# Optimization experiments

Hardware: AMD Instinct MI355X
Metric: run time of the kernel (lower is better)

The kernel has to match this reference:

```python
import jax, jax.numpy as jnp
import numpy as np

B, T, S, D_MODEL = 2, 16, 512, 768
N_HEADS, HEAD_DIM = 12, 64
N_LATENTS = 32


def build_encoder_mask(modality_ids, n_latents):
    # encoder mode: latent queries attend everything; non-latent queries attend same-modality only
    S = modality_ids.shape[0]
    is_q_lat = (jnp.arange(S) < n_latents)[:, None]            # (S,1)
    same_mod = modality_ids[:, None] == modality_ids[None, :]  # (S,S)
    return jnp.where(is_q_lat, True, same_mod)                 # (S,S) bool


def setup_inputs() -> dict:
    key = jax.random.key(0)
    ks = jax.random.split(key, 9)
    x = jax.random.normal(ks[0], (B, T, S, D_MODEL), jnp.float32)
    w_scale = 1.0 / np.sqrt(D_MODEL)
    # flax MultiHeadDotProductAttention param layout: qkv kernels (D, H, head_dim), out kernel (H, head_dim, D)
    Wq = jax.random.normal(ks[1], (D_MODEL, N_HEADS, HEAD_DIM), jnp.float32) * w_scale
    Wk = jax.random.normal(ks[2], (D_MODEL, N_HEADS, HEAD_DIM), jnp.float32) * w_scale
    Wv = jax.random.normal(ks[3], (D_MODEL, N_HEADS, HEAD_DIM), jnp.float32) * w_scale
    Wo = jax.random.normal(ks[4], (N_HEADS, HEAD_DIM, D_MODEL), jnp.float32) * w_scale
    bq = jnp.zeros((N_HEADS, HEAD_DIM), jnp.float32)
    bk = jnp.zeros((N_HEADS, HEAD_DIM), jnp.float32)
    bv = jnp.zeros((N_HEADS, HEAD_DIM), jnp.float32)
    bo = jnp.zeros((D_MODEL,), jnp.float32)
    # 32 latent tokens (id -1), then 240 tokens of modality 0 and 240 of modality 1
    modality_ids = jnp.concatenate([
        jnp.full((N_LATENTS,), -1, jnp.int32),
        jnp.zeros((240,), jnp.int32),
        jnp.ones((240,), jnp.int32),
    ])
    return dict(x=x, Wq=Wq, bq=bq, Wk=Wk, bk=bk, Wv=Wv, bv=bv, Wo=Wo, bo=bo,
                modality_ids=modality_ids, n_latents=N_LATENTS)


def reference(x, Wq, bq, Wk, bk, Wv, bv, Wo, bo, modality_ids, n_latents):
    B, T, S, D = x.shape
    H, hd = Wq.shape[1], Wq.shape[2]
    xf = x.reshape(B * T, S, D)                                   # (BT,S,D)
    q = (jnp.einsum('bsd,dhk->bshk', xf, Wq) + bq) / jnp.sqrt(jnp.asarray(hd, x.dtype))
    k = jnp.einsum('bsd,dhk->bshk', xf, Wk) + bk
    v = jnp.einsum('bsd,dhk->bshk', xf, Wv) + bv
    scores = jnp.einsum('bqhd,bkhd->bhqk', q, k)                  # (BT,H,S,S)
    mask = build_encoder_mask(modality_ids, n_latents)            # (S,S)
    neg = jnp.finfo(x.dtype).min
    scores = jnp.where(mask[None, None], scores, neg)
    attn = jax.nn.softmax(scores, axis=-1)
    ctx = jnp.einsum('bhqk,bkhd->bqhd', attn, v)                  # (BT,S,H,hd)
    y = jnp.einsum('bqhd,hdo->bqo', ctx, Wo) + bo                 # (BT,S,D)
    return y.reshape(B, T, S, D)
```

## Files before the change

kernel.cpp:

```cpp
#include <hip/hip_runtime.h>
#include <stdint.h>

#define BT_N  32
#define SEQL  512
#define DM    768
#define NHEAD 12
#define HDIM  64
#define MTOT  (BT_N * SEQL)

typedef __bf16 bf16x8 __attribute__((ext_vector_type(8)));
typedef float  f32x4  __attribute__((ext_vector_type(4)));

__device__ __forceinline__ float b2f(uint16_t u)  { return __uint_as_float(((uint32_t)u) << 16); }
__device__ __forceinline__ uint16_t f2b(float f) {
    uint32_t u = __float_as_uint(f);
    return (uint16_t)((u + 0x7fffu + ((u >> 16) & 1u)) >> 16);
}
__device__ __forceinline__ void split_bf16(float x, uint16_t& hi, uint16_t& lo) {
    hi = f2b(x);
    lo = f2b(x - b2f(hi));
}

__device__ __forceinline__ void gload16(const void* g, void* l) {
    __builtin_amdgcn_global_load_lds(
        (const __attribute__((address_space(1))) void*)g,
        (__attribute__((address_space(3))) void*)l,
        16, 0, 0);
}

__global__ __launch_bounds__(256) void split_x_kernel(
    const float* __restrict__ X, uint16_t* __restrict__ Xh, uint16_t* __restrict__ Xl)
{
    size_t i = ((size_t)blockIdx.x * 256 + threadIdx.x) * 4;
    float4 v = *(const float4*)(X + i);
    float xx[4] = {v.x, v.y, v.z, v.w};
    ushort4 h, l;
    uint16_t hh, ll;
    split_bf16(xx[0], hh, ll); h.x = hh; l.x = ll;
    split_bf16(xx[1], hh, ll); h.y = hh; l.y = ll;
    split_bf16(xx[2], hh, ll); h.z = hh; l.z = ll;
    split_bf16(xx[3], hh, ll); h.w = hh; l.w = ll;
    *(ushort4*)(Xh + i) = h;
    *(ushort4*)(Xl + i) = l;
}

__global__ __launch_bounds__(256) void wprep_kernel(
    const float* __restrict__ Wq, const float* __restrict__ Wk,
    const float* __restrict__ Wv, const float* __restrict__ Wo,
    uint16_t* __restrict__ WqTh, uint16_t* __restrict__ WqTl,
    uint16_t* __restrict__ WkTh, uint16_t* __restrict__ WkTl,
    uint16_t* __restrict__ WvT,  uint16_t* __restrict__ WoT)
{
    __shared__ float tile[32][33];
    const int z = blockIdx.z;
    const float* W; uint16_t* Th; uint16_t* Tl;
    if (z == 0)      { W = Wq; Th = WqTh; Tl = WqTl; }
    else if (z == 1) { W = Wk; Th = WkTh; Tl = WkTl; }
    else if (z == 2) { W = Wv; Th = WvT;  Tl = nullptr; }
    else             { W = Wo; Th = WoT;  Tl = nullptr; }

    const int k0 = blockIdx.x * 32, n0 = blockIdx.y * 32;
    const int tid = threadIdx.x;
    {
        int r = tid >> 3, c = (tid & 7) * 4;
        *(float4*)&tile[r][c] = *(const float4*)(W + (size_t)(k0 + r) * DM + n0 + c);
    }
    __syncthreads();
    {
        int nl = tid >> 3, kk = (tid & 7) * 4;
        ushort4 h, l;
        uint16_t hh, ll;
        float v0 = tile[kk + 0][nl], v1 = tile[kk + 1][nl];
        float v2 = tile[kk + 2][nl], v3 = tile[kk + 3][nl];
        split_bf16(v0, hh, ll); h.x = hh; l.x = ll;
        split_bf16(v1, hh, ll); h.y = hh; l.y = ll;
        split_bf16(v2, hh, ll); h.z = hh; l.z = ll;
        split_bf16(v3, hh, ll); h.w = hh; l.w = ll;
        size_t o = (size_t)(n0 + nl) * DM + k0 + kk;
        *(ushort4*)(Th + o) = h;
        if (Tl) *(ushort4*)(Tl + o) = l;
    }
}

__global__ __launch_bounds__(256, 2) void qk_gemm_split(
    const uint16_t* __restrict__ Xh, const uint16_t* __restrict__ Xl,
    const uint16_t* __restrict__ WqTh, const uint16_t* __restrict__ WqTl,
    const uint16_t* __restrict__ WkTh, const uint16_t* __restrict__ WkTl,
    const float* __restrict__ bq, const float* __restrict__ bk,
    uint16_t* __restrict__ Qh, uint16_t* __restrict__ Ql,
    uint16_t* __restrict__ Kh, uint16_t* __restrict__ Kl)
{
    __shared__ uint16_t lds[2][16384];

    const int m0 = blockIdx.x * 128;
    const int n0 = blockIdx.y * 128;
    const int z  = blockIdx.z;

    const uint16_t* Bh_g = z ? WkTh : WqTh;
    const uint16_t* Bl_g = z ? WkTl : WqTl;
    const float* bias    = z ? bk : bq;
    uint16_t* OutH       = z ? Kh : Qh;
    uint16_t* OutL       = z ? Kl : Ql;
    const float scale    = z ? 1.0f : 0.125f;

    const int tid  = threadIdx.x;
    const int lane = tid & 63, wave = tid >> 6;
    const int quad = lane >> 4, l16 = lane & 15;
    const int wm = (wave >> 1) * 64, wn = (wave & 1) * 64;

    const uint16_t* src[8];
    #pragma unroll
    for (int i = 0; i < 8; i++) {
        int d    = (i * 256 + tid) * 16;
        int row  = (d >> 7) & 127;
        int colb = d & 127;
        int scol = colb ^ ((row & 7) << 4);
        int kofs = (scol & 63) >> 1;
        const uint16_t* g;
        if (d < 16384) g = (scol < 64 ? Xh : Xl)     + (size_t)(m0 + row) * DM + kofs;
        else           g = (scol < 64 ? Bh_g : Bl_g) + (size_t)(n0 + row) * DM + kofs;
        src[i] = g;
    }

    int offA[4], offB[4];
    #pragma unroll
    for (int i = 0; i < 4; i++) {
        int r  = wm + i * 16 + l16;
        offA[i] = r * 64 + (((quad * 16) ^ ((r & 7) << 4)) >> 1);
        int rb = wn + i * 16 + l16;
        offB[i] = 8192 + rb * 64 + (((quad * 16) ^ ((rb & 7) << 4)) >> 1);
    }

    f32x4 acc[4][4];
    #pragma unroll
    for (int i = 0; i < 4; i++)
        #pragma unroll
        for (int j = 0; j < 4; j++) acc[i][j] = (f32x4){0.f,0.f,0.f,0.f};

    auto stage = [&](int buf) {
        #pragma unroll
        for (int i = 0; i < 8; i++) {
            gload16(src[i], &lds[buf][(i * 256 + wave * 64) * 8]);
            src[i] += 32;
        }
    };
    auto computeTile = [&](int buf) {
        const uint16_t* base = &lds[buf][0];
        bf16x8 ah[4], al[4], bh[4], bl[4];
        #pragma unroll
        for (int i = 0; i < 4; i++) {
            ah[i] = *(const bf16x8*)(base + offA[i]);
            al[i] = *(const bf16x8*)(base + (offA[i] ^ 32));
            bh[i] = *(const bf16x8*)(base + offB[i]);
            bl[i] = *(const bf16x8*)(base + (offB[i] ^ 32));
        }
        #pragma unroll
        for (int mi = 0; mi < 4; mi++)
            #pragma unroll
            for (int ni = 0; ni < 4; ni++) {
                acc[mi][ni] = __builtin_amdgcn_mfma_f32_16x16x32_bf16(al[mi], bh[ni], acc[mi][ni], 0, 0, 0);
                acc[mi][ni] = __builtin_amdgcn_mfma_f32_16x16x32_bf16(ah[mi], bl[ni], acc[mi][ni], 0, 0, 0);
                acc[mi][ni] = __builtin_amdgcn_mfma_f32_16x16x32_bf16(ah[mi], bh[ni], acc[mi][ni], 0, 0, 0);
            }
    };

    stage(0);
    asm volatile("s_waitcnt vmcnt(0)" ::: "memory");
    __syncthreads();

    int cur = 0;
    for (int t = 0; t < 23; t++) {
        stage(cur ^ 1);
        computeTile(cur);
        asm volatile("s_waitcnt vmcnt(0)" ::: "memory");
        __syncthreads();
        cur ^= 1;
    }
    computeTile(cur);

    #pragma unroll
    for (int i = 0; i < 4; i++) {
        #pragma unroll
        for (int j = 0; j < 4; j++) {
            int n = n0 + wn + j * 16 + l16;
            float bsv = bias[n];
            int hh = n >> 6, dd = n & 63;
            int mb = m0 + wm + i * 16 + quad * 4;
            #pragma unroll
            for (int r = 0; r < 4; r++) {
                int m = mb + r;
                float val = (acc[i][j][r] + bsv) * scale;
                uint16_t vh, vl; split_bf16(val, vh, vl);
                int bt = m >> 9, s = m & 511;
                size_t idx = (((size_t)bt * NHEAD + hh) * SEQL + s) * HDIM + dd;
                OutH[idx] = vh; OutL[idx] = vl;
            }
        }
    }
}

__global__ __launch_bounds__(256, 2) void v_gemm_plain(
    const uint16_t* __restrict__ Xh, const uint16_t* __restrict__ WvT,
    const float* __restrict__ bv, uint16_t* __restrict__ Vt)
{
    __shared__ uint16_t lds[2][16384];

    const int m0 = blockIdx.x * 128;
    const int n0 = blockIdx.y * 128;
    const int tid  = threadIdx.x;
    const int lane = tid & 63, wave = tid >> 6;
    const int quad = lane >> 4, l16 = lane & 15;
    const int wm = (wave >> 1) * 64, wn = (wave & 1) * 64;

    const uint16_t* src[8];
    #pragma unroll
    for (int i = 0; i < 8; i++) {
        int d    = (i * 256 + tid) * 16;
        int row  = (d >> 7) & 127;
        int colb = d & 127;
        int scol = colb ^ ((row & 7) << 4);
        int kofs = scol >> 1;
        src[i] = (d < 16384 ? Xh + (size_t)(m0 + row) * DM
                            : WvT + (size_t)(n0 + row) * DM) + kofs;
    }

    int offA[4], offB[4];
    #pragma unroll
    for (int i = 0; i < 4; i++) {
        int r  = wm + i * 16 + l16;
        offA[i] = r * 64 + (((quad * 16) ^ ((r & 7) << 4)) >> 1);
        int rb = wn + i * 16 + l16;
        offB[i] = 8192 + rb * 64 + (((quad * 16) ^ ((rb & 7) << 4)) >> 1);
    }

    f32x4 acc[4][4];
    #pragma unroll
    for (int i = 0; i < 4; i++)
        #pragma unroll
        for (int j = 0; j < 4; j++) acc[i][j] = (f32x4){0.f,0.f,0.f,0.f};

    auto stage = [&](int buf) {
        #pragma unroll
        for (int i = 0; i < 8; i++) {
            gload16(src[i], &lds[buf][(i * 256 + wave * 64) * 8]);
            src[i] += 64;
        }
    };
    auto computeTile = [&](int buf) {
        const uint16_t* base = &lds[buf][0];
        bf16x8 a0[4], a1[4], b0[4], b1[4];
        #pragma unroll
        for (int i = 0; i < 4; i++) {
            a0[i] = *(const bf16x8*)(base + offA[i]);
            a1[i] = *(const bf16x8*)(base + (offA[i] ^ 32));
            b0[i] = *(const bf16x8*)(base + offB[i]);
            b1[i] = *(const bf16x8*)(base + (offB[i] ^ 32));
        }
        #pragma unroll
        for (int mi = 0; mi < 4; mi++)
            #pragma unroll
            for (int ni = 0; ni < 4; ni++)
                acc[mi][ni] = __builtin_amdgcn_mfma_f32_16x16x32_bf16(a0[mi], b0[ni], acc[mi][ni], 0, 0, 0);
        #pragma unroll
        for (int mi = 0; mi < 4; mi++)
            #pragma unroll
            for (int ni = 0; ni < 4; ni++)
                acc[mi][ni] = __builtin_amdgcn_mfma_f32_16x16x32_bf16(a1[mi], b1[ni], acc[mi][ni], 0, 0, 0);
    };

    stage(0);
    asm volatile("s_waitcnt vmcnt(0)" ::: "memory");
    __syncthreads();

    int cur = 0;
    for (int t = 0; t < 11; t++) {
        stage(cur ^ 1);
        computeTile(cur);
        asm volatile("s_waitcnt vmcnt(0)" ::: "memory");
        __syncthreads();
        cur ^= 1;
    }
    computeTile(cur);

    #pragma unroll
    for (int i = 0; i < 4; i++) {
        #pragma unroll
        for (int j = 0; j < 4; j++) {
            int n = n0 + wn + j * 16 + l16;
            float bsv = bv[n];
            int hh = n >> 6, dd = n & 63;
            int mb = m0 + wm + i * 16 + quad * 4;
            int bt = mb >> 9, sb = mb & 511;
            ushort4 pk;
            pk.x = f2b(acc[i][j][0] + bsv);
            pk.y = f2b(acc[i][j][1] + bsv);
            pk.z = f2b(acc[i][j][2] + bsv);
            pk.w = f2b(acc[i][j][3] + bsv);
            *(ushort4*)&Vt[(((size_t)bt * NHEAD + hh) * HDIM + dd) * SEQL + sb] = pk;
        }
    }
}

__global__ __launch_bounds__(256, 2) void out_proj_v3(
    const uint16_t* __restrict__ A, const uint16_t* __restrict__ WoT,
    const float* __restrict__ bias, float* __restrict__ Y)
{
    __shared__ uint16_t lds[2][16384];

    const int m0 = blockIdx.x * 128;
    const int n0 = blockIdx.y * 128;
    const int tid  = threadIdx.x;
    const int lane = tid & 63, wave = tid >> 6;
    const int quad = lane >> 4, l16 = lane & 15;
    const int wm = (wave >> 1) * 64, wn = (wave & 1) * 64;

    const uint16_t* src[8];
    #pragma unroll
    for (int i = 0; i < 8; i++) {
        int d    = (i * 256 + tid) * 16;
        int row  = (d >> 7) & 127;
        int colb = d & 127;
        int scol = colb ^ ((row & 7) << 4);
        int kofs = scol >> 1;
        src[i] = (d < 16384 ? A + (size_t)(m0 + row) * DM
                            : WoT + (size_t)(n0 + row) * DM) + kofs;
    }

    int offA[4], offB[4];
    #pragma unroll
    for (int i = 0; i < 4; i++) {
        int r  = wm + i * 16 + l16;
        offA[i] = r * 64 + (((quad * 16) ^ ((r & 7) << 4)) >> 1);
        int rb = wn + i * 16 + l16;
        offB[i] = 8192 + rb * 64 + (((quad * 16) ^ ((rb & 7) << 4)) >> 1);
    }

    f32x4 acc[4][4];
    #pragma unroll
    for (int i = 0; i < 4; i++)
        #pragma unroll
        for (int j = 0; j < 4; j++) acc[i][j] = (f32x4){0.f,0.f,0.f,0.f};

    auto stage = [&](int buf) {
        #pragma unroll
        for (int i = 0; i < 8; i++) {
            gload16(src[i], &lds[buf][(i * 256 + wave * 64) * 8]);
            src[i] += 64;
        }
    };
    auto computeTile = [&](int buf) {
        const uint16_t* base = &lds[buf][0];
        bf16x8 a0[4], a1[4], b0[4], b1[4];
        #pragma unroll
        for (int i = 0; i < 4; i++) {
            a0[i] = *(const bf16x8*)(base + offA[i]);
            a1[i] = *(const bf16x8*)(base + (offA[i] ^ 32));
            b0[i] = *(const bf16x8*)(base + offB[i]);
            b1[i] = *(const bf16x8*)(base + (offB[i] ^ 32));
        }
        #pragma unroll
        for (int mi = 0; mi < 4; mi++)
            #pragma unroll
            for (int ni = 0; ni < 4; ni++)
                acc[mi][ni] = __builtin_amdgcn_mfma_f32_16x16x32_bf16(a0[mi], b0[ni], acc[mi][ni], 0, 0, 0);
        #pragma unroll
        for (int mi = 0; mi < 4; mi++)
            #pragma unroll
            for (int ni = 0; ni < 4; ni++)
                acc[mi][ni] = __builtin_amdgcn_mfma_f32_16x16x32_bf16(a1[mi], b1[ni], acc[mi][ni], 0, 0, 0);
    };

    stage(0);
    asm volatile("s_waitcnt vmcnt(0)" ::: "memory");
    __syncthreads();

    int cur = 0;
    for (int t = 0; t < 11; t++) {
        stage(cur ^ 1);
        computeTile(cur);
        asm volatile("s_waitcnt vmcnt(0)" ::: "memory");
        __syncthreads();
        cur ^= 1;
    }
    computeTile(cur);

    #pragma unroll
    for (int i = 0; i < 4; i++) {
        #pragma unroll
        for (int j = 0; j < 4; j++) {
            int n = n0 + wn + j * 16 + l16;
            float bsv = bias[n];
            int mb = m0 + wm + i * 16 + quad * 4;
            #pragma unroll
            for (int r = 0; r < 4; r++)
                Y[(size_t)(mb + r) * DM + n] = acc[i][j][r] + bsv;
        }
    }
}

#define QTILE 64

__global__ __launch_bounds__(256) void attn_mfma_v2(
    const uint16_t* __restrict__ Qhg, const uint16_t* __restrict__ Qlg,
    const uint16_t* __restrict__ Khg, const uint16_t* __restrict__ Klg,
    const uint16_t* __restrict__ Vtg, const int* __restrict__ modality,
    const int* __restrict__ nlat_p, uint16_t* __restrict__ ctx)
{
    __shared__ uint16_t KhS[64][72];
    __shared__ uint16_t KlS[64][72];
    __shared__ uint16_t Vs[64][72];
    __shared__ __bf16   Ps[QTILE][72];
    __shared__ int modk_s[64];

    const int bh = blockIdx.x;
    const int bt = bh / NHEAD, h = bh % NHEAD;
    const int q0 = blockIdx.y * QTILE;
    const int tid = threadIdx.x, lane = tid & 63, wave = tid >> 6;
    const int quad = lane >> 4, l16 = lane & 15;
    const int wq = wave * 16;

    const size_t hb = (size_t)bh * SEQL * HDIM;
    const int nlat = nlat_p[0];

    unsigned needmask;
    {
        int rm = modality[q0 + lane];
        bool hasLat = __any((q0 + lane) < nlat);
        bool has0   = __any(rm == 0);
        bool has1   = __any(rm == 1);
        needmask = 0;
        #pragma unroll
        for (int t8 = 0; t8 < 8; t8++) {
            int km = modality[t8 * 64 + lane];
            bool kb0 = __any(km == 0);
            bool kb1 = __any(km == 1);
            bool need = hasLat || (has0 && kb0) || (has1 && kb1);
            needmask |= (need ? 1u : 0u) << t8;
        }
    }

    bf16x8 qh[2], ql[2];
    #pragma unroll
    for (int ks = 0; ks < 2; ks++) {
        size_t o = hb + (size_t)(q0 + wq + l16) * HDIM + ks*32 + quad*8;
        qh[ks] = *(const bf16x8*)(Qhg + o);
        ql[ks] = *(const bf16x8*)(Qlg + o);
    }

    int  mq[4]; bool lat_[4];
    #pragma unroll
    for (int r = 0; r < 4; r++) {
        int row = q0 + wq + quad*4 + r;
        mq[r]   = modality[row];
        lat_[r] = row < nlat;
    }

    float mrow[4], lrow[4];
    #pragma unroll
    for (int r = 0; r < 4; r++) { mrow[r] = -3e38f; lrow[r] = 0.f; }
    f32x4 O[4];
    #pragma unroll
    for (int dt = 0; dt < 4; dt++) O[dt] = (f32x4){0.f,0.f,0.f,0.f};

    for (int t8 = 0; t8 < 8; t8++) {
        if (!(needmask & (1u << t8))) continue;
        const int s0 = t8 * 64;
        __syncthreads();
        {
            int rr = tid >> 2, c0 = (tid & 3) * 16;
            const uint16_t* kp = Khg + hb + (size_t)(s0 + rr) * HDIM + c0;
            const uint16_t* lp = Klg + hb + (size_t)(s0 + rr) * HDIM + c0;
            const uint16_t* vp = Vtg + hb + (size_t)rr * SEQL + s0 + c0;
            *(uint4*)&KhS[rr][c0]     = *(const uint4*)kp;
            *(uint4*)&KhS[rr][c0 + 8] = *((const uint4*)kp + 1);
            *(uint4*)&KlS[rr][c0]     = *(const uint4*)lp;
            *(uint4*)&KlS[rr][c0 + 8] = *((const uint4*)lp + 1);
            *(uint4*)&Vs[rr][c0]      = *(const uint4*)vp;
            *(uint4*)&Vs[rr][c0 + 8]  = *((const uint4*)vp + 1);
        }
        if (tid < 64) modk_s[tid] = modality[s0 + tid];
        __syncthreads();

        f32x4 S[4];
        #pragma unroll
        for (int n = 0; n < 4; n++) S[n] = (f32x4){0.f,0.f,0.f,0.f};
        __builtin_amdgcn_s_setprio(1);
        #pragma unroll
        for (int n = 0; n < 4; n++) {
            #pragma unroll
            for (int ks = 0; ks < 2; ks++) {
                bf16x8 kh = *(const bf16x8*)&KhS[n*16 + l16][ks*32 + quad*8];
                bf16x8 kl = *(const bf16x8*)&KlS[n*16 + l16][ks*32 + quad*8];
                S[n] = __builtin_amdgcn_mfma_f32_16x16x32_bf16(ql[ks], kh, S[n], 0, 0, 0);
                S[n] = __builtin_amdgcn_mfma_f32_16x16x32_bf16(qh[ks], kl, S[n], 0, 0, 0);
                S[n] = __builtin_amdgcn_mfma_f32_16x16x32_bf16(qh[ks], kh, S[n], 0, 0, 0);
            }
        }
        __builtin_amdgcn_s_setprio(0);

        int mk[4];
        #pragma unroll
        for (int n = 0; n < 4; n++) mk[n] = modk_s[n*16 + l16];
        #pragma unroll
        for (int n = 0; n < 4; n++)
            #pragma unroll
            for (int r = 0; r < 4; r++)
                if (!(lat_[r] || (mq[r] == mk[n]))) S[n][r] = -3e38f;

        float mc4[4], need = 0.f;
        #pragma unroll
        for (int r = 0; r < 4; r++) {
            float mc = fmaxf(fmaxf(S[0][r], S[1][r]), fmaxf(S[2][r], S[3][r]));
            #pragma unroll
            for (int off = 1; off <= 8; off <<= 1)
                mc = fmaxf(mc, __shfl_xor(mc, off, 64));
            mc4[r] = mc;
            need = fmaxf(need, mc - mrow[r]);
        }
        if (__any(need > 8.0f)) {
            #pragma unroll
            for (int r = 0; r < 4; r++) {
                float mn = fmaxf(mrow[r], mc4[r]);
                float al = __expf(mrow[r] - mn);
                mrow[r] = mn;
                lrow[r] *= al;
                #pragma unroll
                for (int dt = 0; dt < 4; dt++) O[dt][r] *= al;
            }
        }
        #pragma unroll
        for (int r = 0; r < 4; r++) {
            float mn = mrow[r];
            float g  = (mn <= -1e37f) ? 0.f : 1.f;
            float sum = 0.f;
            #pragma unroll
            for (int n = 0; n < 4; n++) {
                float p = __expf(S[n][r] - mn) * g;
                Ps[wq + quad*4 + r][n*16 + l16] = (__bf16)p;
                sum += p;
            }
            #pragma unroll
            for (int off = 1; off <= 8; off <<= 1)
                sum += __shfl_xor(sum, off, 64);
            lrow[r] += sum;
        }

        __builtin_amdgcn_s_setprio(1);
        #pragma unroll
        for (int ks = 0; ks < 2; ks++) {
            bf16x8 pa = *(const bf16x8*)&Ps[wq + l16][ks*32 + quad*8];
            #pragma unroll
            for (int dt = 0; dt < 4; dt++) {
                bf16x8 vb = *(const bf16x8*)&Vs[dt*16 + l16][ks*32 + quad*8];
                O[dt] = __builtin_amdgcn_mfma_f32_16x16x32_bf16(pa, vb, O[dt], 0, 0, 0);
            }
        }
        __builtin_amdgcn_s_setprio(0);
    }

    {
        float inv[4];
        #pragma unroll
        for (int r = 0; r < 4; r++) inv[r] = 1.0f / fmaxf(lrow[r], 1e-30f);
        __bf16* ctxb = (__bf16*)ctx;
        #pragma unroll
        for (int dt = 0; dt < 4; dt++) {
            #pragma unroll
            for (int r = 0; r < 4; r++) {
                int row = q0 + wq + quad*4 + r;
                ctxb[(size_t)(bt * SEQL + row) * DM + h*HDIM + dt*16 + l16] =
                    (__bf16)(O[dt][r] * inv[r]);
            }
        }
    }
}

extern "C" void kernel_launch(void* const* d_in, const int* in_sizes, int n_in,
                              void* d_out, int out_size, void* d_ws, size_t ws_size,
                              hipStream_t stream) {
    const float* X  = (const float*)d_in[0];
    const float* Wq = (const float*)d_in[1];
    const float* bq = (const float*)d_in[2];
    const float* Wk = (const float*)d_in[3];
    const float* bk = (const float*)d_in[4];
    const float* Wv = (const float*)d_in[5];
    const float* bv = (const float*)d_in[6];
    const float* Wo = (const float*)d_in[7];
    const float* bo = (const float*)d_in[8];
    const int* modality = (const int*)d_in[9];
    const int* nlat     = (const int*)d_in[10];

    const size_t per = (size_t)MTOT * DM;
    const size_t wsz = (size_t)DM * DM;
    uint16_t* p = (uint16_t*)d_ws;
    uint16_t* Xh   = p; p += per;
    uint16_t* Xl   = p; p += per;
    uint16_t* WqTh = p; p += wsz;
    uint16_t* WqTl = p; p += wsz;
    uint16_t* WkTh = p; p += wsz;
    uint16_t* WkTl = p; p += wsz;
    uint16_t* WvT  = p; p += wsz;
    uint16_t* WoT  = p; p += wsz;
    uint16_t* Qh   = p; p += per;
    uint16_t* Ql   = p; p += per;
    uint16_t* Kh   = p; p += per;
    uint16_t* Kl   = p; p += per;
    uint16_t* Vt   = p; p += per;
    uint16_t* c_ws = Xh;

    split_x_kernel<<<dim3(per / 1024), 256, 0, stream>>>(X, Xh, Xl);
    wprep_kernel<<<dim3(DM / 32, DM / 32, 4), 256, 0, stream>>>(
        Wq, Wk, Wv, Wo, WqTh, WqTl, WkTh, WkTl, WvT, WoT);
    qk_gemm_split<<<dim3(MTOT / 128, DM / 128, 2), 256, 0, stream>>>(
        Xh, Xl, WqTh, WqTl, WkTh, WkTl, bq, bk, Qh, Ql, Kh, Kl);
    v_gemm_plain<<<dim3(MTOT / 128, DM / 128), 256, 0, stream>>>(
        Xh, WvT, bv, Vt);
    attn_mfma_v2<<<dim3(BT_N * NHEAD, SEQL / QTILE), 256, 0, stream>>>(
        Qh, Ql, Kh, Kl, Vt, modality, nlat, c_ws);
    out_proj_v3<<<dim3(MTOT / 128, DM / 128), 256, 0, stream>>>(
        c_ws, WoT, bo, (float*)d_out);
}
```

Measured before the change: 396.0 us.

## Triple-buffer QK GEMM pipeline and remap GEMM blocks for XCD locality

The QK split-bf16 GEMM moves from double to triple buffering in LDS. It uses partial vmcnt waits and raw s_barrier so that two tiles of global loads stay in flight while a third is computed, and launch bounds drop to one block per CU. All three GEMMs switch to a 1D grid with a remap that assigns contiguous work groups to each of the 8 XCDs, aiming at better L2 reuse of the A and B tiles. The costs are 96KB of LDS per block, lower occupancy, and more intricate synchronisation.

```diff
diff --git a/kernel.cpp b/kernel.cpp
--- a/kernel.cpp
+++ b/kernel.cpp
@@ -82,7 +82,7 @@
     }
 }
 
-__global__ __launch_bounds__(256, 2) void qk_gemm_split(
+__global__ __launch_bounds__(256, 1) void qk_gemm_v5(
     const uint16_t* __restrict__ Xh, const uint16_t* __restrict__ Xl,
     const uint16_t* __restrict__ WqTh, const uint16_t* __restrict__ WqTl,
     const uint16_t* __restrict__ WkTh, const uint16_t* __restrict__ WkTl,
@@ -90,11 +90,14 @@
     uint16_t* __restrict__ Qh, uint16_t* __restrict__ Ql,
     uint16_t* __restrict__ Kh, uint16_t* __restrict__ Kl)
 {
-    __shared__ uint16_t lds[2][16384];
-
-    const int m0 = blockIdx.x * 128;
-    const int n0 = blockIdx.y * 128;
-    const int z  = blockIdx.z;
+    __shared__ uint16_t lds[3][16384];
+
+    const int bid = blockIdx.x;
+    const int wg  = (bid & 7) * 192 + (bid >> 3);
+    const int m0  = (wg / 12) * 128;
+    const int yz  = wg % 12;
+    const int n0  = (yz >> 1) * 128;
+    const int z   = yz & 1;
 
     const uint16_t* Bh_g = z ? WkTh : WqTh;
     const uint16_t* Bl_g = z ? WkTl : WqTl;
@@ -165,17 +168,26 @@
     };
 
     stage(0);
+    stage(1);
+    int cur = 0, stg = 2;
+    #pragma unroll 1
+    for (int t = 0; t < 22; t++) {
+        stage(stg); stg = (stg == 2) ? 0 : stg + 1;
+        asm volatile("s_waitcnt vmcnt(16)" ::: "memory");
+        __builtin_amdgcn_s_barrier();
+        computeTile(cur); cur = (cur == 2) ? 0 : cur + 1;
+        asm volatile("s_waitcnt lgkmcnt(0)" ::: "memory");
+        __builtin_amdgcn_sched_barrier(0);
+        __builtin_amdgcn_s_barrier();
+    }
+    asm volatile("s_waitcnt vmcnt(8)" ::: "memory");
+    __builtin_amdgcn_s_barrier();
+    computeTile(cur); cur = (cur == 2) ? 0 : cur + 1;
+    asm volatile("s_waitcnt lgkmcnt(0)" ::: "memory");
+    __builtin_amdgcn_sched_barrier(0);
+    __builtin_amdgcn_s_barrier();
     asm volatile("s_waitcnt vmcnt(0)" ::: "memory");
-    __syncthreads();
-
-    int cur = 0;
-    for (int t = 0; t < 23; t++) {
-        stage(cur ^ 1);
-        computeTile(cur);
-        asm volatile("s_waitcnt vmcnt(0)" ::: "memory");
-        __syncthreads();
-        cur ^= 1;
-    }
+    __builtin_amdgcn_s_barrier();
     computeTile(cur);
 
     #pragma unroll
@@ -205,8 +217,11 @@
 {
     __shared__ uint16_t lds[2][16384];
 
-    const int m0 = blockIdx.x * 128;
-    const int n0 = blockIdx.y * 128;
+    const int bid = blockIdx.x;
+    const int wg  = (bid & 7) * 96 + (bid >> 3);
+    const int m0  = (wg / 6) * 128;
+    const int n0  = (wg % 6) * 128;
+
     const int tid  = threadIdx.x;
     const int lane = tid & 63, wave = tid >> 6;
     const int quad = lane >> 4, l16 = lane & 15;
@@ -307,8 +322,11 @@
 {
     __shared__ uint16_t lds[2][16384];
 
-    const int m0 = blockIdx.x * 128;
-    const int n0 = blockIdx.y * 128;
+    const int bid = blockIdx.x;
+    const int wg  = (bid & 7) * 96 + (bid >> 3);
+    const int m0  = (wg / 6) * 128;
+    const int n0  = (wg % 6) * 128;
+
     const int tid  = threadIdx.x;
     const int lane = tid & 63, wave = tid >> 6;
     const int quad = lane >> 4, l16 = lane & 15;
@@ -611,12 +629,12 @@
     split_x_kernel<<<dim3(per / 1024), 256, 0, stream>>>(X, Xh, Xl);
     wprep_kernel<<<dim3(DM / 32, DM / 32, 4), 256, 0, stream>>>(
         Wq, Wk, Wv, Wo, WqTh, WqTl, WkTh, WkTl, WvT, WoT);
-    qk_gemm_split<<<dim3(MTOT / 128, DM / 128, 2), 256, 0, stream>>>(
+    qk_gemm_v5<<<dim3(1536), 256, 0, stream>>>(
         Xh, Xl, WqTh, WqTl, WkTh, WkTl, bq, bk, Qh, Ql, Kh, Kl);
-    v_gemm_plain<<<dim3(MTOT / 128, DM / 128), 256, 0, stream>>>(
+    v_gemm_plain<<<dim3(768), 256, 0, stream>>>(
         Xh, WvT, bv, Vt);
     attn_mfma_v2<<<dim3(BT_N * NHEAD, SEQL / QTILE), 256, 0, stream>>>(
         Qh, Ql, Kh, Kl, Vt, modality, nlat, c_ws);
-    out_proj_v3<<<dim3(MTOT / 128, DM / 128), 256, 0, stream>>>(
+    out_proj_v3<<<dim3(768), 256, 0, stream>>>(
         c_ws, WoT, bo, (float*)d_out);
 }
```

After: 423.9 us. 7.1% more time.
